# Kernel optimization log

Hardware: AMD Instinct MI355X
Metric: run time of the kernel (lower is better)

Reference implementation:

```python
import jax, jax.numpy as jnp
import numpy as np

D_OUT = 256  # out_channels; fourier dim F = D_OUT (Wr has F/2 rows)

def _fourier_pos(H, W, Wr, w1, b1, w2, b2):
    # normalized (H,W) grid in [-1,1], shape [L,2]
    ys = jnp.linspace(-1.0, 1.0, H)
    xs = jnp.linspace(-1.0, 1.0, W)
    gy, gx = jnp.meshgrid(ys, xs, indexing='ij')
    grid = jnp.stack([gy, gx], axis=-1).reshape(-1, 2)  # [L,2]
    proj = grid @ Wr.T                                   # [L,F/2]
    F = 2 * Wr.shape[0]
    feats = jnp.concatenate([jnp.cos(proj), jnp.sin(proj)], axis=-1) / jnp.sqrt(jnp.float32(F))
    h = jax.nn.gelu(feats @ w1.T + b1)
    return h @ w2.T + b2                                 # [L,D_OUT]

def setup_inputs() -> dict:
    key = jax.random.key(0)
    ks = jax.random.split(key, 11)
    N, D, H, W = 16, 256, 128, 128
    s = 1.0 / np.sqrt(D)
    return {
        'x': jax.random.normal(ks[0], (N, D, H, W), jnp.float32),
        'query': jax.random.normal(ks[1], (D_OUT,), jnp.float32),
        'k_w': jax.random.normal(ks[2], (D_OUT, D), jnp.float32) * s,
        'k_b': jax.random.normal(ks[3], (D_OUT,), jnp.float32) * 0.01,
        'v_w': jax.random.normal(ks[4], (D_OUT, D), jnp.float32) * s,
        'v_b': jax.random.normal(ks[5], (D_OUT,), jnp.float32) * 0.01,
        'Wr': jax.random.normal(ks[6], (D_OUT // 2, 2), jnp.float32),
        'w1': jax.random.normal(ks[7], (D_OUT, D_OUT), jnp.float32) * (1.0 / np.sqrt(D_OUT)),
        'b1': jax.random.normal(ks[8], (D_OUT,), jnp.float32) * 0.01,
        'w2': jax.random.normal(ks[9], (D_OUT, D_OUT), jnp.float32) * (1.0 / np.sqrt(D_OUT)),
        'b2': jax.random.normal(ks[10], (D_OUT,), jnp.float32) * 0.01,
    }

def reference(x, query, k_w, k_b, v_w, v_b, Wr, w1, b1, w2, b2):
    N, D, H, W = x.shape
    L = H * W
    tok = x.reshape(N, D, L).transpose(0, 2, 1)          # [N,L,D]
    pos = _fourier_pos(H, W, Wr, w1, b1, w2, b2)         # [L,D_OUT]
    K = tok @ k_w.T + k_b + pos[None]                    # [N,L,D_OUT]
    V = tok @ v_w.T + v_b                                # [N,L,D_OUT]
    scores = jnp.einsum('nld,d->nl', K, query) / jnp.sqrt(jnp.float32(query.shape[0]))
    attn = jax.nn.softmax(scores, axis=1)                # [N,L]
    return jnp.einsum('nl,nld->nd', attn, V)             # [N,D_OUT]
```

## Files before the change

kernel.cpp:

```cpp
#include <hip/hip_runtime.h>
#include <math.h>

#define NB 16
#define DD 256
#define LL 16384
#define DO 256

#define WS_QKP   0
#define WS_QW2P  2048
#define WS_W1T   4096
#define WS_VWT   (WS_W1T + 65536)
#define WS_PQ    (WS_VWT + 65536)
#define WS_M     (WS_PQ + LL)
#define WS_DEN   (WS_M + NB*32)
#define WS_NUM   (WS_DEN + NB*32)

__device__ __forceinline__ float gelu_tanh(float u) {
    float u3 = u*u*u;
    return 0.5f*u*(1.0f + tanhf(0.7978845608028654f*(u + 0.044715f*u3)));
}

__global__ __launch_bounds__(256) void k0(const float* __restrict__ query,
        const float* __restrict__ k_w, const float* __restrict__ w2,
        const float* __restrict__ w1, const float* __restrict__ v_w,
        float* __restrict__ ws) {
    int t = threadIdx.x, b = blockIdx.x;
    if (b < 16) {
        bool is_k = (b < 8);
        int c = b & 7;
        const float* M = is_k ? k_w : w2;
        float a = 0.f;
        #pragma unroll
        for (int oi = 0; oi < 32; ++oi) {
            int o = c*32 + oi;
            a += M[o*DD + t] * query[o];
        }
        ws[(is_k ? WS_QKP : WS_QW2P) + c*256 + t] = a;
    } else if (b < 272) {
        int f = b - 16;
        ws[WS_W1T + f*DO + t] = w1[t*DO + f];
    } else {
        int d = b - 272;
        ws[WS_VWT + d*DO + t] = v_w[t*DD + d];
    }
}

__global__ __launch_bounds__(256) void k1_pq(const float* __restrict__ Wr,
        const float* __restrict__ b1, float* __restrict__ ws) {
    __shared__ __align__(16) float featsT[256*36];
    __shared__ __align__(16) float wbuf[32*256];
    int t = threadIdx.x;
    int w = t >> 6, lane = t & 63;
    int l0 = blockIdx.x * 32;
    int r = t & 127;
    float wr0 = Wr[r*2], wr1 = Wr[r*2+1];
    bool is_cos = (t < 128);
    #pragma unroll 8
    for (int lr = 0; lr < 32; ++lr) {
        int l = l0 + lr;
        int i = l >> 7, j = l & 127;
        float y = -1.0f + (2.0f/127.0f)*(float)i;
        float xg = -1.0f + (2.0f/127.0f)*(float)j;
        float p = y*wr0 + xg*wr1;
        featsT[t*36 + lr] = (is_cos ? cosf(p) : sinf(p)) * 0.0625f;
    }
    int o4 = lane * 4;
    float z[8][4];
    #pragma unroll
    for (int a = 0; a < 8; ++a) { z[a][0]=0.f; z[a][1]=0.f; z[a][2]=0.f; z[a][3]=0.f; }
    float4 qwv; qwv.x = 0.f; qwv.y = 0.f; qwv.z = 0.f; qwv.w = 0.f;
    #pragma unroll
    for (int c = 0; c < 8; ++c) {
        float4 p = *(const float4*)(ws + WS_QW2P + c*256 + o4);
        qwv.x += p.x; qwv.y += p.y; qwv.z += p.z; qwv.w += p.w;
    }
    for (int fc = 0; fc < 8; ++fc) {
        #pragma unroll
        for (int i2 = 0; i2 < 8; ++i2) {
            int idx = i2*256 + t;
            int fl = idx >> 6;
            int c = (idx & 63) * 4;
            *(float4*)(wbuf + fl*256 + c) =
                *(const float4*)(ws + WS_W1T + (fc*32+fl)*DO + c);
        }
        __syncthreads();
        for (int fl = 0; fl < 32; ++fl) {
            float4 wv = *(const float4*)(wbuf + fl*256 + o4);
            const float* fr = featsT + (fc*32+fl)*36 + w*8;
            float4 fa = *(const float4*)(fr);
            float4 fb = *(const float4*)(fr+4);
            float fv[8] = {fa.x,fa.y,fa.z,fa.w,fb.x,fb.y,fb.z,fb.w};
            #pragma unroll
            for (int lr = 0; lr < 8; ++lr) {
                z[lr][0] += fv[lr]*wv.x; z[lr][1] += fv[lr]*wv.y;
                z[lr][2] += fv[lr]*wv.z; z[lr][3] += fv[lr]*wv.w;
            }
        }
        __syncthreads();
    }
    float4 b1v = *(const float4*)(b1 + o4);
    #pragma unroll
    for (int lr = 0; lr < 8; ++lr) {
        float pp = gelu_tanh(z[lr][0]+b1v.x)*qwv.x + gelu_tanh(z[lr][1]+b1v.y)*qwv.y
                 + gelu_tanh(z[lr][2]+b1v.z)*qwv.z + gelu_tanh(z[lr][3]+b1v.w)*qwv.w;
        for (int off = 32; off > 0; off >>= 1) pp += __shfl_xor(pp, off);
        if (lane == 0) ws[WS_PQ + l0 + w*8 + lr] = pp;
    }
}

__global__ __launch_bounds__(256) void k2_main(const float* __restrict__ x,
        float* __restrict__ ws) {
    __shared__ __align__(16) float tile[DD*65];
    __shared__ float qk_s[DD];
    __shared__ float e_s[64];
    __shared__ float part[256];
    __shared__ float m_s, den_s, sc_s;
    int t = threadIdx.x;
    int n = blockIdx.x >> 5, lb = blockIdx.x & 31;
    const float* xb = x + (size_t)n * DD * LL;
    float aqk = 0.f;
    #pragma unroll
    for (int c = 0; c < 8; ++c) aqk += ws[WS_QKP + c*256 + t];
    qk_s[t] = aqk;
    if (t == 0) { m_s = -INFINITY; den_s = 0.f; sc_s = 0.f; }
    float num = 0.f;
    int w = t >> 6, lane = t & 63;
    int dld = t >> 4;
    int li = (t & 15) * 4;
    float4 v[16];
    #pragma unroll
    for (int i2 = 0; i2 < 16; ++i2)
        v[i2] = *(const float4*)(xb + (size_t)(i2*16 + dld)*LL + lb*512 + li);
    __syncthreads();
    #pragma unroll
    for (int i2 = 0; i2 < 16; ++i2) {
        float* dst = tile + (i2*16 + dld)*65 + li;
        dst[0]=v[i2].x; dst[1]=v[i2].y; dst[2]=v[i2].z; dst[3]=v[i2].w;
    }
    __syncthreads();
    for (int tb = 0; tb < 8; ++tb) {
        int l0 = lb*512 + tb*64;
        if (tb < 7) {
            int l0n = l0 + 64;
            #pragma unroll
            for (int i2 = 0; i2 < 16; ++i2)
                v[i2] = *(const float4*)(xb + (size_t)(i2*16 + dld)*LL + l0n + li);
        }
        float acc = 0.f;
        int dbase = w*64;
        #pragma unroll 8
        for (int i2 = 0; i2 < 64; ++i2)
            acc += tile[(dbase+i2)*65 + lane] * qk_s[dbase+i2];
        part[t] = acc;
        __syncthreads();
        if (t < 64) {
            float dot = part[t] + part[64+t] + part[128+t] + part[192+t];
            float score = (dot + ws[WS_PQ + l0 + t]) * 0.0625f;
            float mc = score;
            for (int off=32; off>0; off>>=1) mc = fmaxf(mc, __shfl_xor(mc, off));
            float mold = m_s;
            float mnew = fmaxf(mold, mc);
            float e = expf(score - mnew);
            e_s[t] = e;
            float dc = e;
            for (int off=32; off>0; off>>=1) dc += __shfl_xor(dc, off);
            if (t == 0) {
                float sc = expf(mold - mnew);
                den_s = den_s*sc + dc;
                m_s = mnew;
                sc_s = sc;
            }
        }
        __syncthreads();
        float sc = sc_s;
        float acc2 = 0.f;
        #pragma unroll 8
        for (int l = 0; l < 64; ++l)
            acc2 += e_s[l] * tile[t*65 + l];
        num = num*sc + acc2;
        __syncthreads();
        if (tb < 7) {
            #pragma unroll
            for (int i2 = 0; i2 < 16; ++i2) {
                float* dst = tile + (i2*16 + dld)*65 + li;
                dst[0]=v[i2].x; dst[1]=v[i2].y; dst[2]=v[i2].z; dst[3]=v[i2].w;
            }
        }
        __syncthreads();
    }
    int pb = n*32 + lb;
    ws[WS_NUM + pb*256 + t] = num;
    if (t == 0) { ws[WS_M + pb] = m_s; ws[WS_DEN + pb] = den_s; }
}

__global__ __launch_bounds__(256) void k3_final(const float* __restrict__ ws,
        const float* __restrict__ v_b, float* __restrict__ out) {
    __shared__ float s_s[DD];
    int t = threadIdx.x, n = blockIdx.x;
    float m = -INFINITY;
    #pragma unroll
    for (int lb = 0; lb < 32; ++lb) m = fmaxf(m, ws[WS_M + n*32 + lb]);
    float den = 0.f;
    #pragma unroll
    for (int lb = 0; lb < 32; ++lb)
        den += ws[WS_DEN + n*32 + lb] * expf(ws[WS_M + n*32 + lb] - m);
    float sacc = 0.f;
    #pragma unroll 4
    for (int lb = 0; lb < 32; ++lb) {
        float sc = expf(ws[WS_M + n*32 + lb] - m);
        sacc += ws[WS_NUM + (n*32+lb)*256 + t] * sc;
    }
    s_s[t] = sacc / den;
    __syncthreads();
    float acc = v_b[t];
    #pragma unroll 8
    for (int d = 0; d < DD; ++d)
        acc += ws[WS_VWT + d*DO + t] * s_s[d];
    out[n*DO + t] = acc;
}

extern "C" void kernel_launch(void* const* d_in, const int* in_sizes, int n_in,
                              void* d_out, int out_size, void* d_ws, size_t ws_size,
                              hipStream_t stream) {
    const float* x     = (const float*)d_in[0];
    const float* query = (const float*)d_in[1];
    const float* k_w   = (const float*)d_in[2];
    const float* v_w   = (const float*)d_in[4];
    const float* v_b   = (const float*)d_in[5];
    const float* Wr    = (const float*)d_in[6];
    const float* w1    = (const float*)d_in[7];
    const float* b1    = (const float*)d_in[8];
    const float* w2    = (const float*)d_in[9];
    float* ws  = (float*)d_ws;
    float* out = (float*)d_out;

    k0<<<528, 256, 0, stream>>>(query, k_w, w2, w1, v_w, ws);
    k1_pq<<<512, 256, 0, stream>>>(Wr, b1, ws);
    k2_main<<<512, 256, 0, stream>>>(x, ws);
    k3_final<<<16, 256, 0, stream>>>(ws, v_b, out);
}
```

Measured before the change: 446.7 us.

## Keep x tiles in registers with double buffering instead of LDS transpose

The main attention kernel no longer stages each 256x64 slice of x through a padded LDS tile. Each thread keeps its float4 slices in registers with a two-deep prefetch buffer. Partial scores are reduced with wave shuffles, and the numerator is accumulated per thread and shuffle-reduced at the end. This removes LDS stores and loads plus two barriers per step, at the cost of much higher register pressure, which may lower occupancy. The final kernel is also split across four blocks per batch to add parallelism to the V projection.

```diff
diff --git a/kernel.cpp b/kernel.cpp
--- a/kernel.cpp
+++ b/kernel.cpp
@@ -110,52 +110,65 @@
 
 __global__ __launch_bounds__(256) void k2_main(const float* __restrict__ x,
         float* __restrict__ ws) {
-    __shared__ __align__(16) float tile[DD*65];
     __shared__ float qk_s[DD];
-    __shared__ float e_s[64];
-    __shared__ float part[256];
+    __shared__ __align__(16) float e_s[64];
+    __shared__ __align__(16) float part[256];
     __shared__ float m_s, den_s, sc_s;
     int t = threadIdx.x;
     int n = blockIdx.x >> 5, lb = blockIdx.x & 31;
-    const float* xb = x + (size_t)n * DD * LL;
+    const float* xb = x + (size_t)n * DD * LL + lb * 512;
+    int dld = t >> 4, li = (t & 15) * 4;
+    int w = t >> 6, lane = t & 63;
+    float4 v[2][16];
+    #pragma unroll
+    for (int i2 = 0; i2 < 16; ++i2)
+        v[0][i2] = *(const float4*)(xb + (size_t)(i2*16 + dld)*LL + li);
     float aqk = 0.f;
     #pragma unroll
     for (int c = 0; c < 8; ++c) aqk += ws[WS_QKP + c*256 + t];
     qk_s[t] = aqk;
     if (t == 0) { m_s = -INFINITY; den_s = 0.f; sc_s = 0.f; }
-    float num = 0.f;
-    int w = t >> 6, lane = t & 63;
-    int dld = t >> 4;
-    int li = (t & 15) * 4;
-    float4 v[16];
-    #pragma unroll
-    for (int i2 = 0; i2 < 16; ++i2)
-        v[i2] = *(const float4*)(xb + (size_t)(i2*16 + dld)*LL + lb*512 + li);
+    float pqv[8];
+    if (t < 64) {
+        #pragma unroll
+        for (int tb = 0; tb < 8; ++tb) pqv[tb] = ws[WS_PQ + lb*512 + tb*64 + t];
+    }
     __syncthreads();
-    #pragma unroll
-    for (int i2 = 0; i2 < 16; ++i2) {
-        float* dst = tile + (i2*16 + dld)*65 + li;
-        dst[0]=v[i2].x; dst[1]=v[i2].y; dst[2]=v[i2].z; dst[3]=v[i2].w;
-    }
-    __syncthreads();
+    float qkr[16];
+    #pragma unroll
+    for (int i2 = 0; i2 < 16; ++i2) qkr[i2] = qk_s[i2*16 + dld];
+    float numacc[16];
+    #pragma unroll
+    for (int i2 = 0; i2 < 16; ++i2) numacc[i2] = 0.f;
+    #pragma unroll
     for (int tb = 0; tb < 8; ++tb) {
-        int l0 = lb*512 + tb*64;
+        const int cur = tb & 1, nxt = cur ^ 1;
         if (tb < 7) {
-            int l0n = l0 + 64;
             #pragma unroll
             for (int i2 = 0; i2 < 16; ++i2)
-                v[i2] = *(const float4*)(xb + (size_t)(i2*16 + dld)*LL + l0n + li);
-        }
-        float acc = 0.f;
-        int dbase = w*64;
-        #pragma unroll 8
-        for (int i2 = 0; i2 < 64; ++i2)
-            acc += tile[(dbase+i2)*65 + lane] * qk_s[dbase+i2];
-        part[t] = acc;
+                v[nxt][i2] = *(const float4*)(xb + (size_t)(i2*16 + dld)*LL
+                                              + (tb+1)*64 + li);
+        }
+        float sp0=0.f, sp1=0.f, sp2=0.f, sp3=0.f;
+        #pragma unroll
+        for (int i2 = 0; i2 < 16; ++i2) {
+            sp0 += v[cur][i2].x * qkr[i2];
+            sp1 += v[cur][i2].y * qkr[i2];
+            sp2 += v[cur][i2].z * qkr[i2];
+            sp3 += v[cur][i2].w * qkr[i2];
+        }
+        sp0 += __shfl_xor(sp0, 16); sp0 += __shfl_xor(sp0, 32);
+        sp1 += __shfl_xor(sp1, 16); sp1 += __shfl_xor(sp1, 32);
+        sp2 += __shfl_xor(sp2, 16); sp2 += __shfl_xor(sp2, 32);
+        sp3 += __shfl_xor(sp3, 16); sp3 += __shfl_xor(sp3, 32);
+        if (lane < 16) {
+            float4 spv; spv.x=sp0; spv.y=sp1; spv.z=sp2; spv.w=sp3;
+            *(float4*)(part + w*64 + li) = spv;
+        }
         __syncthreads();
         if (t < 64) {
             float dot = part[t] + part[64+t] + part[128+t] + part[192+t];
-            float score = (dot + ws[WS_PQ + l0 + t]) * 0.0625f;
+            float score = (dot + pqv[tb]) * 0.0625f;
             float mc = score;
             for (int off=32; off>0; off>>=1) mc = fmaxf(mc, __shfl_xor(mc, off));
             float mold = m_s;
@@ -173,50 +186,61 @@
         }
         __syncthreads();
         float sc = sc_s;
-        float acc2 = 0.f;
-        #pragma unroll 8
-        for (int l = 0; l < 64; ++l)
-            acc2 += e_s[l] * tile[t*65 + l];
-        num = num*sc + acc2;
-        __syncthreads();
-        if (tb < 7) {
-            #pragma unroll
-            for (int i2 = 0; i2 < 16; ++i2) {
-                float* dst = tile + (i2*16 + dld)*65 + li;
-                dst[0]=v[i2].x; dst[1]=v[i2].y; dst[2]=v[i2].z; dst[3]=v[i2].w;
-            }
-        }
-        __syncthreads();
+        float4 e4 = *(const float4*)(e_s + li);
+        #pragma unroll
+        for (int i2 = 0; i2 < 16; ++i2) {
+            numacc[i2] = numacc[i2]*sc
+                + e4.x*v[cur][i2].x + e4.y*v[cur][i2].y
+                + e4.z*v[cur][i2].z + e4.w*v[cur][i2].w;
+        }
+    }
+    #pragma unroll
+    for (int i2 = 0; i2 < 16; ++i2) {
+        float nv = numacc[i2];
+        nv += __shfl_xor(nv, 1); nv += __shfl_xor(nv, 2);
+        nv += __shfl_xor(nv, 4); nv += __shfl_xor(nv, 8);
+        numacc[i2] = nv;
     }
     int pb = n*32 + lb;
-    ws[WS_NUM + pb*256 + t] = num;
+    if ((t & 15) == 0) {
+        #pragma unroll
+        for (int i2 = 0; i2 < 16; ++i2)
+            ws[WS_NUM + pb*256 + i2*16 + dld] = numacc[i2];
+    }
     if (t == 0) { ws[WS_M + pb] = m_s; ws[WS_DEN + pb] = den_s; }
 }
 
 __global__ __launch_bounds__(256) void k3_final(const float* __restrict__ ws,
         const float* __restrict__ v_b, float* __restrict__ out) {
     __shared__ float s_s[DD];
-    int t = threadIdx.x, n = blockIdx.x;
+    __shared__ float part[256];
+    int t = threadIdx.x;
+    int n = blockIdx.x >> 2, oq = blockIdx.x & 3;
     float m = -INFINITY;
     #pragma unroll
     for (int lb = 0; lb < 32; ++lb) m = fmaxf(m, ws[WS_M + n*32 + lb]);
-    float den = 0.f;
-    #pragma unroll
-    for (int lb = 0; lb < 32; ++lb)
-        den += ws[WS_DEN + n*32 + lb] * expf(ws[WS_M + n*32 + lb] - m);
-    float sacc = 0.f;
+    float den = 0.f, sacc = 0.f;
     #pragma unroll 4
     for (int lb = 0; lb < 32; ++lb) {
         float sc = expf(ws[WS_M + n*32 + lb] - m);
+        den += ws[WS_DEN + n*32 + lb] * sc;
         sacc += ws[WS_NUM + (n*32+lb)*256 + t] * sc;
     }
     s_s[t] = sacc / den;
     __syncthreads();
-    float acc = v_b[t];
+    int w = t >> 6, lane = t & 63;
+    int o = oq*64 + lane;
+    float acc = 0.f;
     #pragma unroll 8
-    for (int d = 0; d < DD; ++d)
-        acc += ws[WS_VWT + d*DO + t] * s_s[d];
-    out[n*DO + t] = acc;
+    for (int i = 0; i < 64; ++i) {
+        int d = w*64 + i;
+        acc += ws[WS_VWT + d*DO + o] * s_s[d];
+    }
+    part[t] = acc;
+    __syncthreads();
+    if (t < 64)
+        out[n*DO + oq*64 + t] = v_b[oq*64 + t]
+            + part[t] + part[64+t] + part[128+t] + part[192+t];
 }
 
 extern "C" void kernel_launch(void* const* d_in, const int* in_sizes, int n_in,
@@ -237,5 +261,5 @@
     k0<<<528, 256, 0, stream>>>(query, k_w, w2, w1, v_w, ws);
     k1_pq<<<512, 256, 0, stream>>>(Wr, b1, ws);
     k2_main<<<512, 256, 0, stream>>>(x, ws);
-    k3_final<<<16, 256, 0, stream>>>(ws, v_b, out);
-}
+    k3_final<<<64, 256, 0, stream>>>(ws, v_b, out);
+}
```

Measured after the change: 450.3 us. No clear change (+0.8%).
